# Kernel optimization log

Hardware: AMD Instinct MI355X
Metric: run time of the kernel (lower is better)

The kernel has to match this reference:

```python
import jax, jax.numpy as jnp
import numpy as np

# The 16 differentiable binary logic gates used by difflogic are all of the form
# c0 + c1*a + c2*b + c3*(a*b). Rows are gate ids 0..15.
GATE_COEF = jnp.array([
    [0., 0., 0., 0.],    # 0: False
    [0., 0., 0., 1.],    # 1: a AND b
    [0., 1., 0., -1.],   # 2: a AND NOT b
    [0., 1., 0., 0.],    # 3: a
    [0., 0., 1., -1.],   # 4: NOT a AND b
    [0., 0., 1., 0.],    # 5: b
    [0., 1., 1., -2.],   # 6: XOR
    [0., 1., 1., -1.],   # 7: OR
    [1., -1., -1., 1.],  # 8: NOR
    [1., -1., -1., 2.],  # 9: XNOR
    [1., 0., -1., 0.],   # 10: NOT b
    [1., 0., -1., 1.],   # 11: a OR NOT b (b implies a)
    [1., -1., 0., 0.],   # 12: NOT a
    [1., -1., 0., 1.],   # 13: NOT a OR b (a implies b)
    [1., 0., 0., -1.],   # 14: NAND
    [1., 0., 0., 0.],    # 15: True
], dtype=jnp.float32)

BATCH = 256
IN_DIM = 1024
WIDTH = 64000
K = 10
TAU = 30.0


def _logic_layer(x, w, idx_a, idx_b):
    # x: [B, in_dim], w: [out, 16], idx_*: [out] int32
    a = x[:, idx_a]            # [B, out]
    b = x[:, idx_b]            # [B, out]
    coef = jax.nn.softmax(w, axis=-1) @ GATE_COEF   # [out, 4]
    return coef[:, 0] + coef[:, 1] * a + coef[:, 2] * b + coef[:, 3] * (a * b)


def setup_inputs() -> dict:
    key = jax.random.key(0)
    ks = jax.random.split(key, 10)
    x = jax.random.uniform(ks[0], (BATCH, IN_DIM), dtype=jnp.float32)
    w1 = jax.random.normal(ks[1], (WIDTH, 16), dtype=jnp.float32)
    w2 = jax.random.normal(ks[2], (WIDTH, 16), dtype=jnp.float32)
    w3 = jax.random.normal(ks[3], (WIDTH, 16), dtype=jnp.float32)
    idx_a1 = jax.random.randint(ks[4], (WIDTH,), 0, IN_DIM, dtype=jnp.int32)
    idx_b1 = jax.random.randint(ks[5], (WIDTH,), 0, IN_DIM, dtype=jnp.int32)
    idx_a2 = jax.random.randint(ks[6], (WIDTH,), 0, WIDTH, dtype=jnp.int32)
    idx_b2 = jax.random.randint(ks[7], (WIDTH,), 0, WIDTH, dtype=jnp.int32)
    idx_a3 = jax.random.randint(ks[8], (WIDTH,), 0, WIDTH, dtype=jnp.int32)
    idx_b3 = jax.random.randint(ks[9], (WIDTH,), 0, WIDTH, dtype=jnp.int32)
    return {"x": x, "w1": w1, "w2": w2, "w3": w3,
            "idx_a1": idx_a1, "idx_b1": idx_b1,
            "idx_a2": idx_a2, "idx_b2": idx_b2,
            "idx_a3": idx_a3, "idx_b3": idx_b3}


def reference(x, w1, w2, w3, idx_a1, idx_b1, idx_a2, idx_b2, idx_a3, idx_b3):
    h = _logic_layer(x, w1, idx_a1, idx_b1)
    h = _logic_layer(h, w2, idx_a2, idx_b2)
    h = _logic_layer(h, w3, idx_a3, idx_b3)
    # GroupSum: [B, WIDTH] -> [B, K, WIDTH//K] -> sum -> / tau
    return h.reshape(h.shape[0], K, -1).sum(axis=-1) / TAU
```

## Files before the change

kernel.cpp:

```cpp
#include <hip/hip_runtime.h>
#include <stdint.h>


#define BATCH   256
#define IN_DIM  1024
#define WIDTH   64000
#define NGROUP  10
#define GSIZE   6400
#define TAU     30.0f
#define NWAVE   16
#define GPB3    256
#define GPW3    (GPB3/NWAVE)
#define NBLK3   (WIDTH/GPB3)
#define BPG     (GSIZE/GPB3)
#define MDW     36

#define TR_BLKS   64
#define COEF_BLKS ((3*WIDTH)/256)
#define SETUP_BLKS (TR_BLKS + COEF_BLKS + 1)

typedef unsigned short ushort_t;

static __device__ __forceinline__ float gate1(float4 c, float a, float b) {
    return fmaf(b, fmaf(c.w, a, c.z), fmaf(c.y, a, c.x));
}
static __device__ __forceinline__ float4 gate4(float4 c, float4 a, float4 b) {
    float4 r;
    r.x = gate1(c, a.x, b.x);
    r.y = gate1(c, a.y, b.y);
    r.z = gate1(c, a.z, b.z);
    r.w = gate1(c, a.w, b.w);
    return r;
}
static __device__ __forceinline__ float ub(uint32_t u, int k) {
    return (float)((u >> (8 * k)) & 0xFFu);
}
static __device__ __forceinline__ float4 gate4b(float4 c, uint32_t a, uint32_t b) {
    float4 r;
    r.x = gate1(c, ub(a, 0), ub(b, 0));
    r.y = gate1(c, ub(a, 1), ub(b, 1));
    r.z = gate1(c, ub(a, 2), ub(b, 2));
    r.w = gate1(c, ub(a, 3), ub(b, 3));
    return r;
}

__global__ __launch_bounds__(256) void setup_kernel(
    const float* __restrict__ x,
    const float* __restrict__ w1, const float* __restrict__ w2,
    const float* __restrict__ w3,
    uint8_t* __restrict__ xT8,
    float4* __restrict__ c1o, float4* __restrict__ c2o, float4* __restrict__ c3o,
    float* __restrict__ out_zero, int out_n)
{
    __shared__ float tile[64][65];
    const int bid = blockIdx.x;
    const int tid = threadIdx.x;

    if (bid < TR_BLKS) {
        const int c0 = (bid & 15) * 64;
        const int b0 = (bid >> 4) * 64;
        const int lt = tid & 63;
        const int wt = tid >> 6;
        for (int r = wt; r < 64; r += 4)
            tile[r][lt] = x[(b0 + r) * IN_DIM + c0 + lt];
        __syncthreads();
        for (int r = wt; r < 64; r += 4) {
            const float v = tile[lt][r];
            xT8[(c0 + r) * BATCH + b0 + lt] =
                (uint8_t)__float2int_rn(v * 255.0f);
        }
        return;
    }
    if (bid == TR_BLKS + COEF_BLKS) {
        for (int i = tid; i < out_n; i += 256) out_zero[i] = 0.f;
        return;
    }

    const int id = (bid - TR_BLKS) * 256 + tid;
    const int layer = id / WIDTH;
    const int j = id - layer * WIDTH;
    const float* w = (layer == 0) ? w1 : (layer == 1) ? w2 : w3;
    float4* cc     = (layer == 0) ? c1o : (layer == 1) ? c2o : c3o;

    const float4* w4 = (const float4*)(w + (size_t)j * 16);
    float4 q0 = w4[0], q1 = w4[1], q2 = w4[2], q3 = w4[3];
    float p[16] = {q0.x,q0.y,q0.z,q0.w, q1.x,q1.y,q1.z,q1.w,
                   q2.x,q2.y,q2.z,q2.w, q3.x,q3.y,q3.z,q3.w};
    float m = p[0];
    #pragma unroll
    for (int i = 1; i < 16; ++i) m = fmaxf(m, p[i]);
    float s = 0.f;
    #pragma unroll
    for (int i = 0; i < 16; ++i) { p[i] = __expf(p[i] - m); s += p[i]; }
    const float inv = 1.0f / s;
    float c0 = (p[8]+p[9]+p[10]+p[11]+p[12]+p[13]+p[14]+p[15]) * inv;
    float c1 = (p[2]+p[3]+p[6]+p[7] - p[8]-p[9]-p[12]-p[13]) * inv;
    float c2 = (p[4]+p[5]+p[6]+p[7] - p[8]-p[9]-p[10]-p[11]) * inv;
    float c3 = (p[1]-p[2]-p[4]-2.f*p[6]-p[7]+p[8]+2.f*p[9]+p[11]+p[13]-p[14]) * inv;
    cc[j] = make_float4(c0, c1, c2, c3);
}

__global__ __launch_bounds__(256) void prep_kernel(
    const int* __restrict__ ia1, const int* __restrict__ ib1,
    const int* __restrict__ ia2, const int* __restrict__ ib2,
    const int* __restrict__ ia3, const int* __restrict__ ib3,
    const float4* __restrict__ c1, const float4* __restrict__ c2,
    const float4* __restrict__ c3,
    int* __restrict__ meta)
{
    const int j = blockIdx.x * 256 + threadIdx.x;
    if (j >= WIDTH) return;

    const int pa = ia3[j], pb = ib3[j];
    const int qaa = ia2[pa], qab = ib2[pa];
    const int qba = ia2[pb], qbb = ib2[pb];

    int* M = meta + (size_t)j * MDW;
    M[0] = ia1[qaa]; M[1] = ib1[qaa];
    M[2] = ia1[qab]; M[3] = ib1[qab];
    M[4] = ia1[qba]; M[5] = ib1[qba];
    M[6] = ia1[qbb]; M[7] = ib1[qbb];

    const float s1 = 1.0f / 255.0f;
    const float s2 = s1 * s1;
    float4* P = (float4*)(M + 8);
    float4 k;
    k = c1[qaa]; P[0] = make_float4(k.x, k.y * s1, k.z * s1, k.w * s2);
    k = c1[qab]; P[1] = make_float4(k.x, k.y * s1, k.z * s1, k.w * s2);
    k = c1[qba]; P[2] = make_float4(k.x, k.y * s1, k.z * s1, k.w * s2);
    k = c1[qbb]; P[3] = make_float4(k.x, k.y * s1, k.z * s1, k.w * s2);
    P[4] = c2[pa];  P[5] = c2[pb];
    P[6] = c3[j];
}

__global__ __launch_bounds__(1024, 4) void fused_kernel(
    const uint8_t* __restrict__ xT8,
    const int*     __restrict__ meta,
    float*         __restrict__ red_out)
{
    __shared__ float4 sred[NWAVE][64];

    const int tid  = threadIdx.x;
    const int lane = tid & 63;
    const int wu   = __builtin_amdgcn_readfirstlane(tid >> 6);
    const int g0   = blockIdx.x * GPB3 + wu * GPW3;

    float4 acc = make_float4(0.f, 0.f, 0.f, 0.f);

    #pragma unroll 2
    for (int i = 0; i < GPW3; ++i) {
        const int g = g0 + i;
        const int* mp = meta + (size_t)g * MDW;
        const int4 iA   = *(const int4*)(mp);
        const int4 iB   = *(const int4*)(mp + 4);

        const uint32_t q0 = ((const uint32_t*)(xT8 + (size_t)iA.x * BATCH))[lane];
        const uint32_t q1 = ((const uint32_t*)(xT8 + (size_t)iA.y * BATCH))[lane];
        const uint32_t q2 = ((const uint32_t*)(xT8 + (size_t)iA.z * BATCH))[lane];
        const uint32_t q3 = ((const uint32_t*)(xT8 + (size_t)iA.w * BATCH))[lane];
        const uint32_t q4 = ((const uint32_t*)(xT8 + (size_t)iB.x * BATCH))[lane];
        const uint32_t q5 = ((const uint32_t*)(xT8 + (size_t)iB.y * BATCH))[lane];
        const uint32_t q6 = ((const uint32_t*)(xT8 + (size_t)iB.z * BATCH))[lane];
        const uint32_t q7 = ((const uint32_t*)(xT8 + (size_t)iB.w * BATCH))[lane];

        const float4 K0 = *(const float4*)(mp + 8);
        const float4 K1 = *(const float4*)(mp + 12);
        const float4 K2 = *(const float4*)(mp + 16);
        const float4 K3 = *(const float4*)(mp + 20);
        const float4 K4 = *(const float4*)(mp + 24);
        const float4 K5 = *(const float4*)(mp + 28);
        const float4 K6 = *(const float4*)(mp + 32);

        const float4 haa = gate4b(K0, q0, q1);
        const float4 hab = gate4b(K1, q2, q3);
        const float4 hba = gate4b(K2, q4, q5);
        const float4 hbb = gate4b(K3, q6, q7);
        const float4 h2a = gate4(K4, haa, hab);
        const float4 h2b = gate4(K5, hba, hbb);
        const float4 h3  = gate4(K6, h2a, h2b);
        acc.x += h3.x; acc.y += h3.y; acc.z += h3.z; acc.w += h3.w;
    }

    sred[wu][lane] = acc;
    __syncthreads();
    if (wu == 0) {
        float4 t = sred[0][lane];
        #pragma unroll
        for (int w = 1; w < NWAVE; ++w) {
            float4 q = sred[w][lane];
            t.x += q.x; t.y += q.y; t.z += q.z; t.w += q.w;
        }
        const float sc = 1.0f / TAU;
        const int grp = blockIdx.x / BPG;
        const int b0 = lane * 4;
        atomicAdd(&red_out[(b0 + 0) * NGROUP + grp], t.x * sc);
        atomicAdd(&red_out[(b0 + 1) * NGROUP + grp], t.y * sc);
        atomicAdd(&red_out[(b0 + 2) * NGROUP + grp], t.z * sc);
        atomicAdd(&red_out[(b0 + 3) * NGROUP + grp], t.w * sc);
    }
}

extern "C" void kernel_launch(void* const* d_in, const int* in_sizes, int n_in,
                              void* d_out, int out_size, void* d_ws, size_t ws_size,
                              hipStream_t stream)
{
    const float* x   = (const float*)d_in[0];
    const float* w1  = (const float*)d_in[1];
    const float* w2  = (const float*)d_in[2];
    const float* w3  = (const float*)d_in[3];
    const int*   ia1 = (const int*)d_in[4];
    const int*   ib1 = (const int*)d_in[5];
    const int*   ia2 = (const int*)d_in[6];
    const int*   ib2 = (const int*)d_in[7];
    const int*   ia3 = (const int*)d_in[8];
    const int*   ib3 = (const int*)d_in[9];
    float* out = (float*)d_out;

    char* ws = (char*)d_ws;
    uint8_t* xT8 = (uint8_t*)ws;
    int*    meta = (int*)(ws + (size_t)IN_DIM * BATCH);
    float4*   c1 = (float4*)(meta + (size_t)WIDTH * MDW);
    float4*   c2 = c1 + WIDTH;
    float4*   c3 = c2 + WIDTH;

    setup_kernel<<<SETUP_BLKS, 256, 0, stream>>>(x, w1, w2, w3, xT8,
                                                 c1, c2, c3, out, out_size);
    prep_kernel<<<WIDTH / 256, 256, 0, stream>>>(ia1, ib1, ia2, ib2, ia3, ib3,
                                                 c1, c2, c3, meta);
    fused_kernel<<<NBLK3, 1024, 0, stream>>>(xT8, meta, out);
}
```

Baseline: 122.2 us.

## Split each wave into two half-waves processing two gates with 8-byte loads

Each wave now handles two output gates per iteration. The low 32 lanes work on one gate and the high 32 on the other, and each lane loads 8 batch bytes (uint2) instead of 4. This halves the loop trip count and makes each gathered load wider, to reduce memory instructions and latency per gate. The cost is more registers (8 accumulators, both gates' coefficients loaded, then selected), a select on every index, and the unroll changed from 2 to 1.

```diff
diff --git a/kernel.cpp b/kernel.cpp
--- a/kernel.cpp
+++ b/kernel.cpp
@@ -24,24 +24,9 @@
 static __device__ __forceinline__ float gate1(float4 c, float a, float b) {
     return fmaf(b, fmaf(c.w, a, c.z), fmaf(c.y, a, c.x));
 }
-static __device__ __forceinline__ float4 gate4(float4 c, float4 a, float4 b) {
-    float4 r;
-    r.x = gate1(c, a.x, b.x);
-    r.y = gate1(c, a.y, b.y);
-    r.z = gate1(c, a.z, b.z);
-    r.w = gate1(c, a.w, b.w);
-    return r;
-}
-static __device__ __forceinline__ float ub(uint32_t u, int k) {
-    return (float)((u >> (8 * k)) & 0xFFu);
-}
-static __device__ __forceinline__ float4 gate4b(float4 c, uint32_t a, uint32_t b) {
-    float4 r;
-    r.x = gate1(c, ub(a, 0), ub(b, 0));
-    r.y = gate1(c, ub(a, 1), ub(b, 1));
-    r.z = gate1(c, ub(a, 2), ub(b, 2));
-    r.w = gate1(c, ub(a, 3), ub(b, 3));
-    return r;
+static __device__ __forceinline__ float ub2(uint2 q, int j) {
+    return (j < 4) ? (float)((q.x >> (8 * j)) & 0xFFu)
+                   : (float)((q.y >> (8 * (j - 4))) & 0xFFu);
 }
 
 __global__ __launch_bounds__(256) void setup_kernel(
@@ -133,70 +118,109 @@
     P[6] = c3[j];
 }
 
+#define TREE_ELEM(j) do {                                                      \
+    const float v0 = ub2(q0, j), v1 = ub2(q1, j);                              \
+    const float v2 = ub2(q2, j), v3 = ub2(q3, j);                              \
+    const float v4 = ub2(q4, j), v5 = ub2(q5, j);                              \
+    const float v6 = ub2(q6, j), v7 = ub2(q7, j);                              \
+    const float haa = gate1(K0, v0, v1);                                       \
+    const float hab = gate1(K1, v2, v3);                                       \
+    const float hba = gate1(K2, v4, v5);                                       \
+    const float hbb = gate1(K3, v6, v7);                                       \
+    const float h2a = gate1(K4, haa, hab);                                     \
+    const float h2b = gate1(K5, hba, hbb);                                     \
+    a##j += gate1(K6, h2a, h2b);                                               \
+} while (0)
+
 __global__ __launch_bounds__(1024, 4) void fused_kernel(
     const uint8_t* __restrict__ xT8,
     const int*     __restrict__ meta,
     float*         __restrict__ red_out)
 {
-    __shared__ float4 sred[NWAVE][64];
+    __shared__ float4 sredA[NWAVE][64];
+    __shared__ float4 sredB[NWAVE][64];
 
     const int tid  = threadIdx.x;
     const int lane = tid & 63;
     const int wu   = __builtin_amdgcn_readfirstlane(tid >> 6);
     const int g0   = blockIdx.x * GPB3 + wu * GPW3;
 
-    float4 acc = make_float4(0.f, 0.f, 0.f, 0.f);
-
-    #pragma unroll 2
-    for (int i = 0; i < GPW3; ++i) {
-        const int g = g0 + i;
-        const int* mp = meta + (size_t)g * MDW;
-        const int4 iA   = *(const int4*)(mp);
-        const int4 iB   = *(const int4*)(mp + 4);
-
-        const uint32_t q0 = ((const uint32_t*)(xT8 + (size_t)iA.x * BATCH))[lane];
-        const uint32_t q1 = ((const uint32_t*)(xT8 + (size_t)iA.y * BATCH))[lane];
-        const uint32_t q2 = ((const uint32_t*)(xT8 + (size_t)iA.z * BATCH))[lane];
-        const uint32_t q3 = ((const uint32_t*)(xT8 + (size_t)iA.w * BATCH))[lane];
-        const uint32_t q4 = ((const uint32_t*)(xT8 + (size_t)iB.x * BATCH))[lane];
-        const uint32_t q5 = ((const uint32_t*)(xT8 + (size_t)iB.y * BATCH))[lane];
-        const uint32_t q6 = ((const uint32_t*)(xT8 + (size_t)iB.z * BATCH))[lane];
-        const uint32_t q7 = ((const uint32_t*)(xT8 + (size_t)iB.w * BATCH))[lane];
-
-        const float4 K0 = *(const float4*)(mp + 8);
-        const float4 K1 = *(const float4*)(mp + 12);
-        const float4 K2 = *(const float4*)(mp + 16);
-        const float4 K3 = *(const float4*)(mp + 20);
-        const float4 K4 = *(const float4*)(mp + 24);
-        const float4 K5 = *(const float4*)(mp + 28);
-        const float4 K6 = *(const float4*)(mp + 32);
-
-        const float4 haa = gate4b(K0, q0, q1);
-        const float4 hab = gate4b(K1, q2, q3);
-        const float4 hba = gate4b(K2, q4, q5);
-        const float4 hbb = gate4b(K3, q6, q7);
-        const float4 h2a = gate4(K4, haa, hab);
-        const float4 h2b = gate4(K5, hba, hbb);
-        const float4 h3  = gate4(K6, h2a, h2b);
-        acc.x += h3.x; acc.y += h3.y; acc.z += h3.z; acc.w += h3.w;
-    }
-
-    sred[wu][lane] = acc;
+    const bool lo  = (lane < 32);
+    const int sub8 = (lane & 31) * 8;
+
+    float a0 = 0.f, a1 = 0.f, a2 = 0.f, a3 = 0.f;
+    float a4 = 0.f, a5 = 0.f, a6 = 0.f, a7 = 0.f;
+
+    #pragma unroll 1
+    for (int i = 0; i < GPW3 / 2; ++i) {
+        const int g = g0 + 2 * i;
+        const int* mpg = meta + (size_t)g * MDW;
+        const int* mph = mpg + MDW;
+        const int4 giA = *(const int4*)(mpg);
+        const int4 giB = *(const int4*)(mpg + 4);
+        const int4 hiA = *(const int4*)(mph);
+        const int4 hiB = *(const int4*)(mph + 4);
+
+        const uint2 q0 = *(const uint2*)(xT8 + (size_t)(lo ? giA.x : hiA.x) * BATCH + sub8);
+        const uint2 q1 = *(const uint2*)(xT8 + (size_t)(lo ? giA.y : hiA.y) * BATCH + sub8);
+        const uint2 q2 = *(const uint2*)(xT8 + (size_t)(lo ? giA.z : hiA.z) * BATCH + sub8);
+        const uint2 q3 = *(const uint2*)(xT8 + (size_t)(lo ? giA.w : hiA.w) * BATCH + sub8);
+        const uint2 q4 = *(const uint2*)(xT8 + (size_t)(lo ? giB.x : hiB.x) * BATCH + sub8);
+        const uint2 q5 = *(const uint2*)(xT8 + (size_t)(lo ? giB.y : hiB.y) * BATCH + sub8);
+        const uint2 q6 = *(const uint2*)(xT8 + (size_t)(lo ? giB.z : hiB.z) * BATCH + sub8);
+        const uint2 q7 = *(const uint2*)(xT8 + (size_t)(lo ? giB.w : hiB.w) * BATCH + sub8);
+
+        const float4 gK0 = *(const float4*)(mpg + 8);
+        const float4 gK1 = *(const float4*)(mpg + 12);
+        const float4 gK2 = *(const float4*)(mpg + 16);
+        const float4 gK3 = *(const float4*)(mpg + 20);
+        const float4 gK4 = *(const float4*)(mpg + 24);
+        const float4 gK5 = *(const float4*)(mpg + 28);
+        const float4 gK6 = *(const float4*)(mpg + 32);
+        const float4 hK0 = *(const float4*)(mph + 8);
+        const float4 hK1 = *(const float4*)(mph + 12);
+        const float4 hK2 = *(const float4*)(mph + 16);
+        const float4 hK3 = *(const float4*)(mph + 20);
+        const float4 hK4 = *(const float4*)(mph + 24);
+        const float4 hK5 = *(const float4*)(mph + 28);
+        const float4 hK6 = *(const float4*)(mph + 32);
+
+        const float4 K0 = lo ? gK0 : hK0;
+        const float4 K1 = lo ? gK1 : hK1;
+        const float4 K2 = lo ? gK2 : hK2;
+        const float4 K3 = lo ? gK3 : hK3;
+        const float4 K4 = lo ? gK4 : hK4;
+        const float4 K5 = lo ? gK5 : hK5;
+        const float4 K6 = lo ? gK6 : hK6;
+
+        TREE_ELEM(0); TREE_ELEM(1); TREE_ELEM(2); TREE_ELEM(3);
+        TREE_ELEM(4); TREE_ELEM(5); TREE_ELEM(6); TREE_ELEM(7);
+    }
+
+    sredA[wu][lane] = make_float4(a0, a1, a2, a3);
+    sredB[wu][lane] = make_float4(a4, a5, a6, a7);
     __syncthreads();
     if (wu == 0) {
-        float4 t = sred[0][lane];
+        float4 tA = sredA[0][lane];
+        float4 tB = sredB[0][lane];
         #pragma unroll
         for (int w = 1; w < NWAVE; ++w) {
-            float4 q = sred[w][lane];
-            t.x += q.x; t.y += q.y; t.z += q.z; t.w += q.w;
+            const float4 pA = sredA[w][lane];
+            const float4 pB = sredB[w][lane];
+            tA.x += pA.x; tA.y += pA.y; tA.z += pA.z; tA.w += pA.w;
+            tB.x += pB.x; tB.y += pB.y; tB.z += pB.z; tB.w += pB.w;
         }
         const float sc = 1.0f / TAU;
         const int grp = blockIdx.x / BPG;
-        const int b0 = lane * 4;
-        atomicAdd(&red_out[(b0 + 0) * NGROUP + grp], t.x * sc);
-        atomicAdd(&red_out[(b0 + 1) * NGROUP + grp], t.y * sc);
-        atomicAdd(&red_out[(b0 + 2) * NGROUP + grp], t.z * sc);
-        atomicAdd(&red_out[(b0 + 3) * NGROUP + grp], t.w * sc);
+        const int b0 = (lane & 31) * 8;
+        atomicAdd(&red_out[(b0 + 0) * NGROUP + grp], tA.x * sc);
+        atomicAdd(&red_out[(b0 + 1) * NGROUP + grp], tA.y * sc);
+        atomicAdd(&red_out[(b0 + 2) * NGROUP + grp], tA.z * sc);
+        atomicAdd(&red_out[(b0 + 3) * NGROUP + grp], tA.w * sc);
+        atomicAdd(&red_out[(b0 + 4) * NGROUP + grp], tB.x * sc);
+        atomicAdd(&red_out[(b0 + 5) * NGROUP + grp], tB.y * sc);
+        atomicAdd(&red_out[(b0 + 6) * NGROUP + grp], tB.z * sc);
+        atomicAdd(&red_out[(b0 + 7) * NGROUP + grp], tB.w * sc);
     }
 }
 
```

After: 138.2 us. 13.1% more time.
